# Kernel optimization log

Hardware: AMD Instinct MI355X
Metric: run time of the kernel (lower is better)

Reference implementation:

```python
import jax, jax.numpy as jnp
import numpy as np

V = 200000  # number of variables (fixed num_segments for aggregation)


def setup_inputs() -> dict:
    key = jax.random.key(0)
    ks = jax.random.split(key, 10)
    E, D, Fe, P = 1000000, 128, 16, 2
    Hm, Hag, Ha = 256, 256, 256  # mem_hidden, mem_agg_hidden, agg_hidden
    Din = D + Fe + 1

    def w(k, shape):
        return jax.random.normal(k, shape, jnp.float32) / jnp.sqrt(shape[1])

    return {
        "variable_state": jax.random.normal(ks[0], (E, D), jnp.float32),
        "edge_feature": jax.random.normal(ks[1], (E, Fe), jnp.float32),
        "solution": jax.random.uniform(ks[2], (V,), jnp.float32),
        "W1m": w(ks[3], (Hm, Din)), "b1m": jnp.zeros((Hm,), jnp.float32),
        "W2m": w(ks[4], (Hag, Hm)),
        "W1a": w(ks[5], (Ha, Hag)), "b1a": jnp.zeros((Ha,), jnp.float32),
        "W2a": w(ks[6], (D, Ha)),
        "Wc": w(ks[7], (P, D)), "bc": jnp.zeros((P,), jnp.float32),
        "variable_index": jax.random.randint(ks[8], (E,), 0, V, jnp.int32),
        "edge_sign": 2 * jax.random.randint(ks[9], (E,), 0, 2, jnp.int32) - 1,
    }


def reference(variable_state, edge_feature, solution, W1m, b1m, W2m, W1a, b1a,
              W2a, Wc, bc, variable_index, edge_sign):
    ls = jax.nn.log_sigmoid
    # per-edge signed solution column: mm(signed_mask, solution) on the sparse incidence
    signed = (edge_sign.astype(jnp.float32) * solution[variable_index])[:, None]  # [E,1]
    x = jnp.concatenate([variable_state, edge_feature, signed], axis=1)  # [E, Din]
    # memory MLP: Linear -> logsigmoid -> Linear -> logsigmoid
    s = ls(ls(x @ W1m.T + b1m) @ W2m.T)  # [E, Hag]
    # aggregation mm(variable_mask, state): sum edges per variable
    agg = jax.ops.segment_sum(s, variable_index, num_segments=V)  # [V, Hag]
    # aggregator MLP
    h = ls(ls(agg @ W1a.T + b1a) @ W2a.T)  # [V, D]
    # variable classifier
    return h @ Wc.T + bc  # [V, P]
```

## Files before the change

### kernel.cpp

```cpp
#include <hip/hip_runtime.h>
#include <hip/hip_bf16.h>

typedef unsigned short u16;
typedef __attribute__((ext_vector_type(8))) short   short8;
typedef __attribute__((ext_vector_type(8))) __bf16  bf16x8;
typedef __attribute__((ext_vector_type(16))) float  floatx16;

#define DD  128
#define FE  16
#define DIN 145
#define K1  160
#define K1P 168
#define HQ  256
#define HQP 264
#define ME  64
#define MV  32

__device__ __forceinline__ float logsig(float x) {
    return fminf(x, 0.f) - __logf(1.f + __expf(-fabsf(x)));
}
__device__ __forceinline__ u16 f2b(float f) {
    union { float f; unsigned u; } x; x.f = f;
    unsigned r = x.u + 0x7fffu + ((x.u >> 16) & 1u);
    return (u16)(r >> 16);
}
__device__ __forceinline__ ushort4 f2b4(float4 v) {
    ushort4 o; o.x = f2b(v.x); o.y = f2b(v.y); o.z = f2b(v.z); o.w = f2b(v.w);
    return o;
}
__device__ __forceinline__ bf16x8 ld_bf8_lds(const short* p) {
    return __builtin_bit_cast(bf16x8, *(const short8*)p);
}
__device__ __forceinline__ bf16x8 ld_bf8_glb(const short* p) {
    return __builtin_bit_cast(bf16x8, *(const short8*)p);
}

__global__ __launch_bounds__(256) void conv_weights(
    const float* __restrict__ W1m, const float* __restrict__ W2m,
    const float* __restrict__ W1a, const float* __restrict__ W2a,
    short* __restrict__ W1mb, short* __restrict__ W2mb,
    short* __restrict__ W1ab, short* __restrict__ W2ab)
{
    int i = blockIdx.x * 256 + threadIdx.x;
    if (i < 256 * K1) {
        int n = i / K1, k = i - n * K1;
        W1mb[i] = (k < DIN) ? (short)f2b(W1m[n * DIN + k]) : (short)0;
    } else if (i < 256 * K1 + 256 * HQ) {
        int j = i - 256 * K1;
        W2mb[j] = (short)f2b(W2m[j]);
    } else if (i < 256 * K1 + 2 * 256 * HQ) {
        int j = i - 256 * K1 - 256 * HQ;
        W1ab[j] = (short)f2b(W1a[j]);
    } else if (i < 256 * K1 + 2 * 256 * HQ + 128 * HQ) {
        int j = i - 256 * K1 - 2 * 256 * HQ;
        W2ab[j] = (short)f2b(W2a[j]);
    }
}

__global__ __launch_bounds__(256) void edge_mfma(
    const float* __restrict__ vs, const float* __restrict__ ef,
    const float* __restrict__ sol, const float* __restrict__ b1m,
    const short* __restrict__ W1mb, const short* __restrict__ W2mb,
    const int* __restrict__ vidx, const int* __restrict__ esign,
    float* __restrict__ agg, int E)
{
    __shared__ short xs[ME][K1P];
    __shared__ short h1s[ME][HQP];
    __shared__ int   vix[ME];
    const int tid = threadIdx.x;
    const int e0 = blockIdx.x * ME;

    for (int i = tid; i < ME * 32; i += 256) {
        int e = i >> 5, q = (i & 31) << 2;
        float4 v = *(const float4*)&vs[(size_t)(e0 + e) * DD + q];
        *(ushort4*)&xs[e][q] = f2b4(v);
    }
    for (int i = tid; i < ME * 4; i += 256) {
        int e = i >> 2, q = (i & 3) << 2;
        float4 v = *(const float4*)&ef[(size_t)(e0 + e) * FE + q];
        *(ushort4*)&xs[e][DD + q] = f2b4(v);
    }
    for (int i = tid; i < ME * 16; i += 256) {
        int e = i >> 4, k = i & 15;
        if (k == 0) {
            int gi = vidx[e0 + e];
            vix[e] = gi;
            xs[e][144] = (short)f2b((float)esign[e0 + e] * sol[gi]);
        } else {
            xs[e][144 + k] = 0;
        }
    }
    __syncthreads();

    const int wv = tid >> 6, lane = tid & 63;
    const int lr = lane & 31, lh = lane >> 5;
    const int n0 = wv * 64;

    floatx16 a00 = {}, a01 = {}, a10 = {}, a11 = {};
    #pragma unroll
    for (int ks = 0; ks < K1 / 16; ++ks) {
        int k = ks * 16 + lh * 8;
        bf16x8 A0 = ld_bf8_lds(&xs[lr][k]);
        bf16x8 A1 = ld_bf8_lds(&xs[32 + lr][k]);
        bf16x8 B0 = ld_bf8_glb(&W1mb[(size_t)(n0 + lr) * K1 + k]);
        bf16x8 B1 = ld_bf8_glb(&W1mb[(size_t)(n0 + 32 + lr) * K1 + k]);
        a00 = __builtin_amdgcn_mfma_f32_32x32x16_bf16(A0, B0, a00, 0, 0, 0);
        a01 = __builtin_amdgcn_mfma_f32_32x32x16_bf16(A0, B1, a01, 0, 0, 0);
        a10 = __builtin_amdgcn_mfma_f32_32x32x16_bf16(A1, B0, a10, 0, 0, 0);
        a11 = __builtin_amdgcn_mfma_f32_32x32x16_bf16(A1, B1, a11, 0, 0, 0);
    }
    {
        float bn0 = b1m[n0 + lr], bn1 = b1m[n0 + 32 + lr];
        #pragma unroll
        for (int r = 0; r < 16; ++r) {
            int row = (r & 3) + 8 * (r >> 2) + 4 * lh;
            h1s[row][n0 + lr]           = (short)f2b(logsig(a00[r] + bn0));
            h1s[row][n0 + 32 + lr]      = (short)f2b(logsig(a01[r] + bn1));
            h1s[32 + row][n0 + lr]      = (short)f2b(logsig(a10[r] + bn0));
            h1s[32 + row][n0 + 32 + lr] = (short)f2b(logsig(a11[r] + bn1));
        }
    }
    __syncthreads();

    a00 = (floatx16){}; a01 = (floatx16){}; a10 = (floatx16){}; a11 = (floatx16){};
    #pragma unroll
    for (int ks = 0; ks < HQ / 16; ++ks) {
        int k = ks * 16 + lh * 8;
        bf16x8 A0 = ld_bf8_lds(&h1s[lr][k]);
        bf16x8 A1 = ld_bf8_lds(&h1s[32 + lr][k]);
        bf16x8 B0 = ld_bf8_glb(&W2mb[(size_t)(n0 + lr) * HQ + k]);
        bf16x8 B1 = ld_bf8_glb(&W2mb[(size_t)(n0 + 32 + lr) * HQ + k]);
        a00 = __builtin_amdgcn_mfma_f32_32x32x16_bf16(A0, B0, a00, 0, 0, 0);
        a01 = __builtin_amdgcn_mfma_f32_32x32x16_bf16(A0, B1, a01, 0, 0, 0);
        a10 = __builtin_amdgcn_mfma_f32_32x32x16_bf16(A1, B0, a10, 0, 0, 0);
        a11 = __builtin_amdgcn_mfma_f32_32x32x16_bf16(A1, B1, a11, 0, 0, 0);
    }
    #pragma unroll
    for (int r = 0; r < 16; ++r) {
        int row = (r & 3) + 8 * (r >> 2) + 4 * lh;
        int va = vix[row], vb = vix[32 + row];
        atomicAdd(&agg[(size_t)va * HQ + n0 + lr],      logsig(a00[r]));
        atomicAdd(&agg[(size_t)va * HQ + n0 + 32 + lr], logsig(a01[r]));
        atomicAdd(&agg[(size_t)vb * HQ + n0 + lr],      logsig(a10[r]));
        atomicAdd(&agg[(size_t)vb * HQ + n0 + 32 + lr], logsig(a11[r]));
    }
}

__global__ __launch_bounds__(256) void var_mfma(
    const float* __restrict__ agg, const float* __restrict__ b1a,
    const short* __restrict__ W1ab, const short* __restrict__ W2ab,
    const float* __restrict__ Wc, const float* __restrict__ bc,
    float* __restrict__ out, int V)
{
    __shared__ short as_s[MV][HQP];
    __shared__ short h1v[MV][HQP];
    __shared__ float hsv[MV][DD + 4];
    const int tid = threadIdx.x;
    const int v0 = blockIdx.x * MV;

    for (int i = tid; i < MV * 64; i += 256) {
        int v = i >> 6, q = (i & 63) << 2;
        float4 a = *(const float4*)&agg[(size_t)(v0 + v) * HQ + q];
        *(ushort4*)&as_s[v][q] = f2b4(a);
    }
    __syncthreads();

    const int wv = tid >> 6, lane = tid & 63;
    const int lr = lane & 31, lh = lane >> 5;
    const int n0 = wv * 64;

    floatx16 c0 = {}, c1 = {};
    #pragma unroll
    for (int ks = 0; ks < HQ / 16; ++ks) {
        int k = ks * 16 + lh * 8;
        bf16x8 A  = ld_bf8_lds(&as_s[lr][k]);
        bf16x8 B0 = ld_bf8_glb(&W1ab[(size_t)(n0 + lr) * HQ + k]);
        bf16x8 B1 = ld_bf8_glb(&W1ab[(size_t)(n0 + 32 + lr) * HQ + k]);
        c0 = __builtin_amdgcn_mfma_f32_32x32x16_bf16(A, B0, c0, 0, 0, 0);
        c1 = __builtin_amdgcn_mfma_f32_32x32x16_bf16(A, B1, c1, 0, 0, 0);
    }
    {
        float bn0 = b1a[n0 + lr], bn1 = b1a[n0 + 32 + lr];
        #pragma unroll
        for (int r = 0; r < 16; ++r) {
            int row = (r & 3) + 8 * (r >> 2) + 4 * lh;
            h1v[row][n0 + lr]      = (short)f2b(logsig(c0[r] + bn0));
            h1v[row][n0 + 32 + lr] = (short)f2b(logsig(c1[r] + bn1));
        }
    }
    __syncthreads();

    floatx16 d0 = {};
    const int n0b = wv * 32;
    #pragma unroll
    for (int ks = 0; ks < HQ / 16; ++ks) {
        int k = ks * 16 + lh * 8;
        bf16x8 A = ld_bf8_lds(&h1v[lr][k]);
        bf16x8 B = ld_bf8_glb(&W2ab[(size_t)(n0b + lr) * HQ + k]);
        d0 = __builtin_amdgcn_mfma_f32_32x32x16_bf16(A, B, d0, 0, 0, 0);
    }
    #pragma unroll
    for (int r = 0; r < 16; ++r) {
        int row = (r & 3) + 8 * (r >> 2) + 4 * lh;
        hsv[row][n0b + lr] = logsig(d0[r]);
    }
    __syncthreads();

    if (tid < MV * 2) {
        int v = tid >> 1, p = tid & 1;
        const float* wrow = Wc + (size_t)p * DD;
        float acc = bc[p];
        for (int k = 0; k < DD; k += 4) {
            float4 w4 = *(const float4*)&wrow[k];
            float4 h4 = *(const float4*)&hsv[v][k];
            acc = fmaf(w4.w, h4.w, fmaf(w4.z, h4.z, fmaf(w4.y, h4.y, fmaf(w4.x, h4.x, acc))));
        }
        out[(size_t)(v0 + v) * 2 + p] = acc;
    }
}

extern "C" void kernel_launch(void* const* d_in, const int* in_sizes, int n_in,
                              void* d_out, int out_size, void* d_ws, size_t ws_size,
                              hipStream_t stream) {
    const float* vs  = (const float*)d_in[0];
    const float* ef  = (const float*)d_in[1];
    const float* sol = (const float*)d_in[2];
    const float* W1m = (const float*)d_in[3];
    const float* b1m = (const float*)d_in[4];
    const float* W2m = (const float*)d_in[5];
    const float* W1a = (const float*)d_in[6];
    const float* b1a = (const float*)d_in[7];
    const float* W2a = (const float*)d_in[8];
    const float* Wc  = (const float*)d_in[9];
    const float* bc  = (const float*)d_in[10];
    const int* vidx  = (const int*)d_in[11];
    const int* sgn   = (const int*)d_in[12];

    const int E = in_sizes[0] / DD;
    const int V = in_sizes[2];

    char* ws = (char*)d_ws;
    float* agg = (float*)ws;
    size_t off = (size_t)V * HQ * sizeof(float);
    short* W1mb = (short*)(ws + off); off += (size_t)256 * K1 * 2;
    short* W2mb = (short*)(ws + off); off += (size_t)256 * HQ * 2;
    short* W1ab = (short*)(ws + off); off += (size_t)256 * HQ * 2;
    short* W2ab = (short*)(ws + off);

    hipMemsetAsync(agg, 0, (size_t)V * HQ * sizeof(float), stream);
    conv_weights<<<dim3(800), dim3(256), 0, stream>>>(
        W1m, W2m, W1a, W2a, W1mb, W2mb, W1ab, W2ab);
    edge_mfma<<<dim3(E / ME), dim3(256), 0, stream>>>(
        vs, ef, sol, b1m, W1mb, W2mb, vidx, sgn, agg, E);
    var_mfma<<<dim3(V / MV), dim3(256), 0, stream>>>(
        agg, b1a, W1ab, W2ab, Wc, bc, (float*)d_out, V);
}
```

Measured before the change: 1.765 ms.

## Sort edges by variable and segment-reduce in block before writing aggregates

Result: slower. 2.183 ms (+23.6%).

```diff
diff --git a/kernel.cpp b/kernel.cpp
--- a/kernel.cpp
+++ b/kernel.cpp
@@ -57,35 +57,94 @@
     }
 }
 
+__global__ __launch_bounds__(256) void hist_kernel(
+    const int* __restrict__ vidx, int* __restrict__ cnt, int E)
+{
+    int e = blockIdx.x * 256 + threadIdx.x;
+    if (e < E) atomicAdd(&cnt[vidx[e]], 1);
+}
+
+#define SCAN_T 1024
+__global__ __launch_bounds__(SCAN_T) void scan_kernel(
+    const int* __restrict__ cnt, int* __restrict__ cursor, int V)
+{
+    __shared__ int part[SCAN_T];
+    const int tid = threadIdx.x;
+    const int chunk = (V + SCAN_T - 1) / SCAN_T;
+    int lo = tid * chunk, hi = lo + chunk;
+    if (lo > V) lo = V;
+    if (hi > V) hi = V;
+    int s = 0;
+    for (int i = lo; i < hi; ++i) s += cnt[i];
+    part[tid] = s;
+    __syncthreads();
+    if (tid == 0) {
+        int run = 0;
+        for (int i = 0; i < SCAN_T; ++i) { int t = part[i]; part[i] = run; run += t; }
+    }
+    __syncthreads();
+    int p = part[tid];
+    for (int i = lo; i < hi; ++i) { int t = cnt[i]; cursor[i] = p; p += t; }
+}
+
+__global__ __launch_bounds__(256) void scatter_kernel(
+    const int* __restrict__ vidx, int* __restrict__ cursor,
+    int* __restrict__ perm, int E)
+{
+    int e = blockIdx.x * 256 + threadIdx.x;
+    if (e < E) {
+        int p = atomicAdd(&cursor[vidx[e]], 1);
+        perm[p] = e;
+    }
+}
+
+template <bool SORTED>
 __global__ __launch_bounds__(256) void edge_mfma(
     const float* __restrict__ vs, const float* __restrict__ ef,
     const float* __restrict__ sol, const float* __restrict__ b1m,
     const short* __restrict__ W1mb, const short* __restrict__ W2mb,
-    const int* __restrict__ vidx, const int* __restrict__ esign,
-    float* __restrict__ agg, int E)
+    const int* __restrict__ perm, const int* __restrict__ vidx,
+    const int* __restrict__ esign, float* __restrict__ agg, int E)
 {
     __shared__ short xs[ME][K1P];
     __shared__ short h1s[ME][HQP];
-    __shared__ int   vix[ME];
+    __shared__ int   eid[ME];
+    __shared__ int   svd[ME];
+    __shared__ int   bflags;
     const int tid = threadIdx.x;
     const int e0 = blockIdx.x * ME;
 
+    if (tid < ME) {
+        int ge;
+        if constexpr (SORTED) ge = perm[e0 + tid]; else ge = e0 + tid;
+        eid[tid] = ge;
+        svd[tid] = vidx[ge];
+    }
+    if constexpr (SORTED) {
+        if (tid == 0) {
+            int f = 0;
+            if (e0 > 0      && vidx[perm[e0 - 1]]  == vidx[perm[e0]])          f |= 1;
+            if (e0 + ME < E && vidx[perm[e0 + ME]] == vidx[perm[e0 + ME - 1]]) f |= 2;
+            bflags = f;
+        }
+    }
+    __syncthreads();
+
     for (int i = tid; i < ME * 32; i += 256) {
         int e = i >> 5, q = (i & 31) << 2;
-        float4 v = *(const float4*)&vs[(size_t)(e0 + e) * DD + q];
+        float4 v = *(const float4*)&vs[(size_t)eid[e] * DD + q];
         *(ushort4*)&xs[e][q] = f2b4(v);
     }
     for (int i = tid; i < ME * 4; i += 256) {
         int e = i >> 2, q = (i & 3) << 2;
-        float4 v = *(const float4*)&ef[(size_t)(e0 + e) * FE + q];
+        float4 v = *(const float4*)&ef[(size_t)eid[e] * FE + q];
         *(ushort4*)&xs[e][DD + q] = f2b4(v);
     }
     for (int i = tid; i < ME * 16; i += 256) {
         int e = i >> 4, k = i & 15;
         if (k == 0) {
-            int gi = vidx[e0 + e];
-            vix[e] = gi;
-            xs[e][144] = (short)f2b((float)esign[e0 + e] * sol[gi]);
+            int ge = eid[e];
+            xs[e][144] = (short)f2b((float)esign[ge] * sol[svd[e]]);
         } else {
             xs[e][144 + k] = 0;
         }
@@ -135,14 +194,61 @@
         a10 = __builtin_amdgcn_mfma_f32_32x32x16_bf16(A1, B0, a10, 0, 0, 0);
         a11 = __builtin_amdgcn_mfma_f32_32x32x16_bf16(A1, B1, a11, 0, 0, 0);
     }
-    #pragma unroll
-    for (int r = 0; r < 16; ++r) {
-        int row = (r & 3) + 8 * (r >> 2) + 4 * lh;
-        int va = vix[row], vb = vix[32 + row];
-        atomicAdd(&agg[(size_t)va * HQ + n0 + lr],      logsig(a00[r]));
-        atomicAdd(&agg[(size_t)va * HQ + n0 + 32 + lr], logsig(a01[r]));
-        atomicAdd(&agg[(size_t)vb * HQ + n0 + lr],      logsig(a10[r]));
-        atomicAdd(&agg[(size_t)vb * HQ + n0 + 32 + lr], logsig(a11[r]));
+
+    if constexpr (SORTED) {
+        __syncthreads();
+        float* h1f = (float*)&h1s[0][0];
+        const int vF = svd[0], vL = svd[ME - 1];
+        const int fl = bflags;
+
+        auto flush = [&](int v, float a) {
+            bool sh = (v == vF && (fl & 1)) || (v == vL && (fl & 2));
+            float* dst = &agg[(size_t)v * HQ + tid];
+            if (sh) atomicAdd(dst, a);
+            else    *dst = a;
+        };
+
+        #pragma unroll
+        for (int r = 0; r < 16; ++r) {
+            int row = (r & 3) + 8 * (r >> 2) + 4 * lh;
+            h1f[row * HQP + n0 + lr]      = logsig(a00[r]);
+            h1f[row * HQP + n0 + 32 + lr] = logsig(a01[r]);
+        }
+        __syncthreads();
+        int cur = -1; float acc = 0.f;
+        for (int r = 0; r < 32; ++r) {
+            int v = svd[r]; float val = h1f[r * HQP + tid];
+            if (v != cur) {
+                if (cur >= 0) flush(cur, acc);
+                cur = v; acc = val;
+            } else acc += val;
+        }
+        __syncthreads();
+        #pragma unroll
+        for (int r = 0; r < 16; ++r) {
+            int row = (r & 3) + 8 * (r >> 2) + 4 * lh;
+            h1f[row * HQP + n0 + lr]      = logsig(a10[r]);
+            h1f[row * HQP + n0 + 32 + lr] = logsig(a11[r]);
+        }
+        __syncthreads();
+        for (int r = 0; r < 32; ++r) {
+            int v = svd[32 + r]; float val = h1f[r * HQP + tid];
+            if (v != cur) {
+                if (cur >= 0) flush(cur, acc);
+                cur = v; acc = val;
+            } else acc += val;
+        }
+        flush(cur, acc);
+    } else {
+        #pragma unroll
+        for (int r = 0; r < 16; ++r) {
+            int row = (r & 3) + 8 * (r >> 2) + 4 * lh;
+            int va = svd[row], vb = svd[32 + row];
+            atomicAdd(&agg[(size_t)va * HQ + n0 + lr],      logsig(a00[r]));
+            atomicAdd(&agg[(size_t)va * HQ + n0 + 32 + lr], logsig(a01[r]));
+            atomicAdd(&agg[(size_t)vb * HQ + n0 + lr],      logsig(a10[r]));
+            atomicAdd(&agg[(size_t)vb * HQ + n0 + 32 + lr], logsig(a11[r]));
+        }
     }
 }
 
@@ -240,18 +346,38 @@
     const int V = in_sizes[2];
 
     char* ws = (char*)d_ws;
-    float* agg = (float*)ws;
-    size_t off = (size_t)V * HQ * sizeof(float);
-    short* W1mb = (short*)(ws + off); off += (size_t)256 * K1 * 2;
-    short* W2mb = (short*)(ws + off); off += (size_t)256 * HQ * 2;
-    short* W1ab = (short*)(ws + off); off += (size_t)256 * HQ * 2;
-    short* W2ab = (short*)(ws + off);
+    size_t off = 0;
+    auto alloc = [&](size_t bytes) {
+        char* p = ws + off;
+        off = (off + bytes + 255) & ~(size_t)255;
+        return p;
+    };
+    float* agg    = (float*)alloc((size_t)V * HQ * sizeof(float));
+    short* W1mb   = (short*)alloc((size_t)256 * K1 * 2);
+    short* W2mb   = (short*)alloc((size_t)256 * HQ * 2);
+    short* W1ab   = (short*)alloc((size_t)256 * HQ * 2);
+    short* W2ab   = (short*)alloc((size_t)128 * HQ * 2);
+    int*   cnt    = (int*)alloc((size_t)V * sizeof(int));
+    int*   cursor = (int*)alloc((size_t)V * sizeof(int));
+    int*   perm   = (int*)alloc((size_t)E * sizeof(int));
+    const bool use_sort = (off <= ws_size);
 
     hipMemsetAsync(agg, 0, (size_t)V * HQ * sizeof(float), stream);
     conv_weights<<<dim3(800), dim3(256), 0, stream>>>(
         W1m, W2m, W1a, W2a, W1mb, W2mb, W1ab, W2ab);
-    edge_mfma<<<dim3(E / ME), dim3(256), 0, stream>>>(
-        vs, ef, sol, b1m, W1mb, W2mb, vidx, sgn, agg, E);
+
+    if (use_sort) {
+        hipMemsetAsync(cnt, 0, (size_t)V * sizeof(int), stream);
+        const int EG = (E + 255) / 256;
+        hist_kernel<<<dim3(EG), dim3(256), 0, stream>>>(vidx, cnt, E);
+        scan_kernel<<<dim3(1), dim3(SCAN_T), 0, stream>>>(cnt, cursor, V);
+        scatter_kernel<<<dim3(EG), dim3(256), 0, stream>>>(vidx, cursor, perm, E);
+        edge_mfma<true><<<dim3(E / ME), dim3(256), 0, stream>>>(
+            vs, ef, sol, b1m, W1mb, W2mb, perm, vidx, sgn, agg, E);
+    } else {
+        edge_mfma<false><<<dim3(E / ME), dim3(256), 0, stream>>>(
+            vs, ef, sol, b1m, W1mb, W2mb, (const int*)nullptr, vidx, sgn, agg, E);
+    }
     var_mfma<<<dim3(V / MV), dim3(256), 0, stream>>>(
         agg, b1a, W1ab, W2ab, Wc, bc, (float*)d_out, V);
 }
```

## Use 8 waves per block with narrower per-wave tiles and swizzled LDS

Applied to the files above, without the earlier changes.

Result: faster. 1.657 ms (-6.1%).

```diff
diff --git a/kernel.cpp b/kernel.cpp
--- a/kernel.cpp
+++ b/kernel.cpp
@@ -15,6 +15,8 @@
 #define HQP 264
 #define ME  64
 #define MV  32
+
+#define H1IDX(r, c) ((((r) * HQ) + (c)) ^ (((r) & 7) << 3))
 
 __device__ __forceinline__ float logsig(float x) {
     return fminf(x, 0.f) - __logf(1.f + __expf(-fabsf(x)));
@@ -57,96 +59,90 @@
     }
 }
 
-__global__ __launch_bounds__(256) void edge_mfma(
+__global__ __launch_bounds__(512, 6) void edge_mfma(
     const float* __restrict__ vs, const float* __restrict__ ef,
     const float* __restrict__ sol, const float* __restrict__ b1m,
     const short* __restrict__ W1mb, const short* __restrict__ W2mb,
     const int* __restrict__ vidx, const int* __restrict__ esign,
     float* __restrict__ agg, int E)
 {
-    __shared__ short xs[ME][K1P];
-    __shared__ short h1s[ME][HQP];
-    __shared__ int   vix[ME];
+    __shared__ short xs[ME * K1P];
+    __shared__ short h1s[ME * HQ];
     const int tid = threadIdx.x;
     const int e0 = blockIdx.x * ME;
 
-    for (int i = tid; i < ME * 32; i += 256) {
+    if (tid < ME) {
+        int ge = e0 + tid;
+        int v  = vidx[ge];
+        *(int*)&xs[tid * K1P + 164] = v;
+        xs[tid * K1P + 144] = (short)f2b((float)esign[ge] * sol[v]);
+        #pragma unroll
+        for (int k = 145; k < K1; ++k) xs[tid * K1P + k] = 0;
+    }
+    for (int i = tid; i < ME * 32; i += 512) {
         int e = i >> 5, q = (i & 31) << 2;
         float4 v = *(const float4*)&vs[(size_t)(e0 + e) * DD + q];
-        *(ushort4*)&xs[e][q] = f2b4(v);
-    }
-    for (int i = tid; i < ME * 4; i += 256) {
+        *(ushort4*)&xs[e * K1P + q] = f2b4(v);
+    }
+    for (int i = tid; i < ME * 4; i += 512) {
         int e = i >> 2, q = (i & 3) << 2;
         float4 v = *(const float4*)&ef[(size_t)(e0 + e) * FE + q];
-        *(ushort4*)&xs[e][DD + q] = f2b4(v);
-    }
-    for (int i = tid; i < ME * 16; i += 256) {
-        int e = i >> 4, k = i & 15;
-        if (k == 0) {
-            int gi = vidx[e0 + e];
-            vix[e] = gi;
-            xs[e][144] = (short)f2b((float)esign[e0 + e] * sol[gi]);
-        } else {
-            xs[e][144 + k] = 0;
-        }
+        *(ushort4*)&xs[e * K1P + DD + q] = f2b4(v);
     }
     __syncthreads();
 
     const int wv = tid >> 6, lane = tid & 63;
     const int lr = lane & 31, lh = lane >> 5;
-    const int n0 = wv * 64;
-
-    floatx16 a00 = {}, a01 = {}, a10 = {}, a11 = {};
-    #pragma unroll
-    for (int ks = 0; ks < K1 / 16; ++ks) {
-        int k = ks * 16 + lh * 8;
-        bf16x8 A0 = ld_bf8_lds(&xs[lr][k]);
-        bf16x8 A1 = ld_bf8_lds(&xs[32 + lr][k]);
-        bf16x8 B0 = ld_bf8_glb(&W1mb[(size_t)(n0 + lr) * K1 + k]);
-        bf16x8 B1 = ld_bf8_glb(&W1mb[(size_t)(n0 + 32 + lr) * K1 + k]);
-        a00 = __builtin_amdgcn_mfma_f32_32x32x16_bf16(A0, B0, a00, 0, 0, 0);
-        a01 = __builtin_amdgcn_mfma_f32_32x32x16_bf16(A0, B1, a01, 0, 0, 0);
-        a10 = __builtin_amdgcn_mfma_f32_32x32x16_bf16(A1, B0, a10, 0, 0, 0);
-        a11 = __builtin_amdgcn_mfma_f32_32x32x16_bf16(A1, B1, a11, 0, 0, 0);
-    }
-    {
-        float bn0 = b1m[n0 + lr], bn1 = b1m[n0 + 32 + lr];
+    const int n0 = wv * 32;
+
+    floatx16 a0 = {}, a1 = {};
+    {
+        const short* Wb = W1mb + (size_t)(n0 + lr) * K1;
+        #pragma unroll 2
+        for (int ks = 0; ks < K1 / 16; ++ks) {
+            int k = ks * 16 + lh * 8;
+            bf16x8 A0 = ld_bf8_lds(&xs[lr * K1P + k]);
+            bf16x8 A1 = ld_bf8_lds(&xs[(32 + lr) * K1P + k]);
+            bf16x8 B  = ld_bf8_glb(&Wb[k]);
+            a0 = __builtin_amdgcn_mfma_f32_32x32x16_bf16(A0, B, a0, 0, 0, 0);
+            a1 = __builtin_amdgcn_mfma_f32_32x32x16_bf16(A1, B, a1, 0, 0, 0);
+        }
+    }
+    {
+        float bn = b1m[n0 + lr];
         #pragma unroll
         for (int r = 0; r < 16; ++r) {
             int row = (r & 3) + 8 * (r >> 2) + 4 * lh;
-            h1s[row][n0 + lr]           = (short)f2b(logsig(a00[r] + bn0));
-            h1s[row][n0 + 32 + lr]      = (short)f2b(logsig(a01[r] + bn1));
-            h1s[32 + row][n0 + lr]      = (short)f2b(logsig(a10[r] + bn0));
-            h1s[32 + row][n0 + 32 + lr] = (short)f2b(logsig(a11[r] + bn1));
-        }
-    }
-    __syncthreads();
-
-    a00 = (floatx16){}; a01 = (floatx16){}; a10 = (floatx16){}; a11 = (floatx16){};
-    #pragma unroll
-    for (int ks = 0; ks < HQ / 16; ++ks) {
-        int k = ks * 16 + lh * 8;
-        bf16x8 A0 = ld_bf8_lds(&h1s[lr][k]);
-        bf16x8 A1 = ld_bf8_lds(&h1s[32 + lr][k]);
-        bf16x8 B0 = ld_bf8_glb(&W2mb[(size_t)(n0 + lr) * HQ + k]);
-        bf16x8 B1 = ld_bf8_glb(&W2mb[(size_t)(n0 + 32 + lr) * HQ + k]);
-        a00 = __builtin_amdgcn_mfma_f32_32x32x16_bf16(A0, B0, a00, 0, 0, 0);
-        a01 = __builtin_amdgcn_mfma_f32_32x32x16_bf16(A0, B1, a01, 0, 0, 0);
-        a10 = __builtin_amdgcn_mfma_f32_32x32x16_bf16(A1, B0, a10, 0, 0, 0);
-        a11 = __builtin_amdgcn_mfma_f32_32x32x16_bf16(A1, B1, a11, 0, 0, 0);
+            h1s[H1IDX(row,      n0 + lr)] = (short)f2b(logsig(a0[r] + bn));
+            h1s[H1IDX(32 + row, n0 + lr)] = (short)f2b(logsig(a1[r] + bn));
+        }
+    }
+    __syncthreads();
+
+    a0 = (floatx16){}; a1 = (floatx16){};
+    {
+        const short* Wb = W2mb + (size_t)(n0 + lr) * HQ;
+        #pragma unroll 2
+        for (int ks = 0; ks < HQ / 16; ++ks) {
+            int k = ks * 16 + lh * 8;
+            bf16x8 A0 = ld_bf8_lds(&h1s[H1IDX(lr,      k)]);
+            bf16x8 A1 = ld_bf8_lds(&h1s[H1IDX(32 + lr, k)]);
+            bf16x8 B  = ld_bf8_glb(&Wb[k]);
+            a0 = __builtin_amdgcn_mfma_f32_32x32x16_bf16(A0, B, a0, 0, 0, 0);
+            a1 = __builtin_amdgcn_mfma_f32_32x32x16_bf16(A1, B, a1, 0, 0, 0);
+        }
     }
     #pragma unroll
     for (int r = 0; r < 16; ++r) {
         int row = (r & 3) + 8 * (r >> 2) + 4 * lh;
-        int va = vix[row], vb = vix[32 + row];
-        atomicAdd(&agg[(size_t)va * HQ + n0 + lr],      logsig(a00[r]));
-        atomicAdd(&agg[(size_t)va * HQ + n0 + 32 + lr], logsig(a01[r]));
-        atomicAdd(&agg[(size_t)vb * HQ + n0 + lr],      logsig(a10[r]));
-        atomicAdd(&agg[(size_t)vb * HQ + n0 + 32 + lr], logsig(a11[r]));
-    }
-}
-
-__global__ __launch_bounds__(256) void var_mfma(
+        int va = *(const int*)&xs[row * K1P + 164];
+        int vb = *(const int*)&xs[(32 + row) * K1P + 164];
+        atomicAdd(&agg[(size_t)va * HQ + n0 + lr], logsig(a0[r]));
+        atomicAdd(&agg[(size_t)vb * HQ + n0 + lr], logsig(a1[r]));
+    }
+}
+
+__global__ __launch_bounds__(512, 6) void var_mfma(
     const float* __restrict__ agg, const float* __restrict__ b1a,
     const short* __restrict__ W1ab, const short* __restrict__ W2ab,
     const float* __restrict__ Wc, const float* __restrict__ bc,
@@ -158,7 +154,7 @@
     const int tid = threadIdx.x;
     const int v0 = blockIdx.x * MV;
 
-    for (int i = tid; i < MV * 64; i += 256) {
+    for (int i = tid; i < MV * 64; i += 512) {
         int v = i >> 6, q = (i & 63) << 2;
         float4 a = *(const float4*)&agg[(size_t)(v0 + v) * HQ + q];
         *(ushort4*)&as_s[v][q] = f2b4(a);
@@ -167,42 +163,45 @@
 
     const int wv = tid >> 6, lane = tid & 63;
     const int lr = lane & 31, lh = lane >> 5;
-    const int n0 = wv * 64;
-
-    floatx16 c0 = {}, c1 = {};
-    #pragma unroll
-    for (int ks = 0; ks < HQ / 16; ++ks) {
-        int k = ks * 16 + lh * 8;
-        bf16x8 A  = ld_bf8_lds(&as_s[lr][k]);
-        bf16x8 B0 = ld_bf8_glb(&W1ab[(size_t)(n0 + lr) * HQ + k]);
-        bf16x8 B1 = ld_bf8_glb(&W1ab[(size_t)(n0 + 32 + lr) * HQ + k]);
-        c0 = __builtin_amdgcn_mfma_f32_32x32x16_bf16(A, B0, c0, 0, 0, 0);
-        c1 = __builtin_amdgcn_mfma_f32_32x32x16_bf16(A, B1, c1, 0, 0, 0);
-    }
-    {
-        float bn0 = b1a[n0 + lr], bn1 = b1a[n0 + 32 + lr];
+    const int n0 = wv * 32;
+
+    floatx16 c0 = {};
+    {
+        const short* Wb = W1ab + (size_t)(n0 + lr) * HQ;
+        #pragma unroll 2
+        for (int ks = 0; ks < HQ / 16; ++ks) {
+            int k = ks * 16 + lh * 8;
+            bf16x8 A = ld_bf8_lds(&as_s[lr][k]);
+            bf16x8 B = ld_bf8_glb(&Wb[k]);
+            c0 = __builtin_amdgcn_mfma_f32_32x32x16_bf16(A, B, c0, 0, 0, 0);
+        }
+    }
+    {
+        float bn = b1a[n0 + lr];
         #pragma unroll
         for (int r = 0; r < 16; ++r) {
             int row = (r & 3) + 8 * (r >> 2) + 4 * lh;
-            h1v[row][n0 + lr]      = (short)f2b(logsig(c0[r] + bn0));
-            h1v[row][n0 + 32 + lr] = (short)f2b(logsig(c1[r] + bn1));
-        }
-    }
-    __syncthreads();
-
-    floatx16 d0 = {};
-    const int n0b = wv * 32;
-    #pragma unroll
-    for (int ks = 0; ks < HQ / 16; ++ks) {
-        int k = ks * 16 + lh * 8;
-        bf16x8 A = ld_bf8_lds(&h1v[lr][k]);
-        bf16x8 B = ld_bf8_glb(&W2ab[(size_t)(n0b + lr) * HQ + k]);
-        d0 = __builtin_amdgcn_mfma_f32_32x32x16_bf16(A, B, d0, 0, 0, 0);
-    }
-    #pragma unroll
-    for (int r = 0; r < 16; ++r) {
-        int row = (r & 3) + 8 * (r >> 2) + 4 * lh;
-        hsv[row][n0b + lr] = logsig(d0[r]);
+            h1v[row][n0 + lr] = (short)f2b(logsig(c0[r] + bn));
+        }
+    }
+    __syncthreads();
+
+    if (wv < 4) {
+        floatx16 d0 = {};
+        const int n0b = wv * 32;
+        const short* Wb = W2ab + (size_t)(n0b + lr) * HQ;
+        #pragma unroll 2
+        for (int ks = 0; ks < HQ / 16; ++ks) {
+            int k = ks * 16 + lh * 8;
+            bf16x8 A = ld_bf8_lds(&h1v[lr][k]);
+            bf16x8 B = ld_bf8_glb(&Wb[k]);
+            d0 = __builtin_amdgcn_mfma_f32_32x32x16_bf16(A, B, d0, 0, 0, 0);
+        }
+        #pragma unroll
+        for (int r = 0; r < 16; ++r) {
+            int row = (r & 3) + 8 * (r >> 2) + 4 * lh;
+            hsv[row][n0b + lr] = logsig(d0[r]);
+        }
     }
     __syncthreads();
 
@@ -250,8 +249,8 @@
     hipMemsetAsync(agg, 0, (size_t)V * HQ * sizeof(float), stream);
     conv_weights<<<dim3(800), dim3(256), 0, stream>>>(
         W1m, W2m, W1a, W2a, W1mb, W2mb, W1ab, W2ab);
-    edge_mfma<<<dim3(E / ME), dim3(256), 0, stream>>>(
+    edge_mfma<<<dim3(E / ME), dim3(512), 0, stream>>>(
         vs, ef, sol, b1m, W1mb, W2mb, vidx, sgn, agg, E);
-    var_mfma<<<dim3(V / MV), dim3(256), 0, stream>>>(
+    var_mfma<<<dim3(V / MV), dim3(512), 0, stream>>>(
         agg, b1a, W1ab, W2ab, Wc, bc, (float*)d_out, V);
 }
```
